# Performance work log

Measured on AMD Instinct MI355X. Metric: run time of the kernel, lower is better.

## Reference

```python
import jax, jax.numpy as jnp
import numpy as np

DIM = 1024
HEAD_DIM = 64
NUM_HEADS = DIM // HEAD_DIM
SCALE = HEAD_DIM ** -0.5
B, N, M = 2, 1024, 2048


def setup_inputs() -> dict:
    key = jax.random.key(0)
    ks = jax.random.split(key, 7)
    x = jax.random.normal(ks[0], (B, N, DIM), dtype=jnp.float32)
    context = jax.random.normal(ks[1], (B, M, DIM), dtype=jnp.float32)
    # query row has at least one valid key (avoids all -inf softmax rows).
    mask = jax.random.bernoulli(ks[2], 0.9, (B, N, M))
    mask = mask.at[:, :, 0].set(True)
    # Linear params (torch nn.Linear convention: y = x @ W.T + b)
    sq = (1.0 / DIM) ** 0.5
    Wq = jax.random.uniform(ks[3], (DIM, DIM), minval=-sq, maxval=sq, dtype=jnp.float32)
    Wkv = jax.random.uniform(ks[4], (2 * DIM, DIM), minval=-sq, maxval=sq, dtype=jnp.float32)
    b_kv = jax.random.uniform(ks[5], (2 * DIM,), minval=-sq, maxval=sq, dtype=jnp.float32)
    Wo = jax.random.uniform(ks[6], (DIM, DIM), minval=-sq, maxval=sq, dtype=jnp.float32)
    return {"x": x, "context": context, "mask": mask,
            "Wq": Wq, "Wkv": Wkv, "b_kv": b_kv, "Wo": Wo}


def reference(x, context, mask, Wq, Wkv, b_kv, Wo):
    b, n, c = x.shape
    m = context.shape[1]
    h, d = NUM_HEADS, HEAD_DIM
    # Q projection (no bias): [b, n, h, d] -> bhnd
    q = (x @ Wq.T).reshape(b, n, h, d).transpose(0, 2, 1, 3)
    # KV projection (with bias): [b, m, 2, h, d]
    kv = (context @ Wkv.T + b_kv).reshape(b, m, 2, h, d)
    k = kv[:, :, 0].transpose(0, 2, 1, 3)  # bhmd
    v = kv[:, :, 1].transpose(0, 2, 1, 3)  # bhmd
    # scores: bhnm, scale applied after matmul as in the original
    attn = jnp.einsum('bhnd,bhmd->bhnm', q, k) * SCALE
    attn = jnp.where(mask[:, None, :, :], attn, -jnp.inf)
    attn = jax.nn.softmax(attn, axis=-1)
    out = jnp.einsum('bhnm,bhmd->bhnd', attn, v)
    out = out.transpose(0, 2, 1, 3).reshape(b, n, h * d)
    return out @ Wo.T
```

## Files before the change

kernel.cpp:

```cpp
#include <hip/hip_runtime.h>


typedef __attribute__((ext_vector_type(8))) short short8;
typedef __attribute__((ext_vector_type(4))) short short4v;
typedef __attribute__((ext_vector_type(4))) float f32x4;
typedef __attribute__((ext_vector_type(4))) int int4v;

#define SCL2E 0.18033688011112042592f

__device__ __forceinline__ float bf2f(short s) {
  unsigned u = ((unsigned)(unsigned short)s) << 16;
  return __uint_as_float(u);
}
__device__ __forceinline__ short f2bf(float f) {
  unsigned u = __float_as_uint(f);
  u += 0x7fffu + ((u >> 16) & 1u);
  return (short)(u >> 16);
}
__device__ __forceinline__ int cvt_pk_bf16(float a, float b) {
  int r;
  asm("v_cvt_pk_bf16_f32 %0, %1, %2" : "=v"(r) : "v"(a), "v"(b));
  return r;
}
__device__ __forceinline__ void gld_lds16(const void* gp, void* lp) {
  __builtin_amdgcn_global_load_lds(
      (const __attribute__((address_space(1))) unsigned int*)gp,
      (__attribute__((address_space(3))) unsigned int*)lp, 16, 0, 0);
}
__device__ __forceinline__ void sbar() {
  __builtin_amdgcn_sched_barrier(0);
  __builtin_amdgcn_s_barrier();
  __builtin_amdgcn_sched_barrier(0);
}
#define WAITVM(N) asm volatile("s_waitcnt vmcnt(" #N ")" ::: "memory")

__device__ __forceinline__ void pipesync() {
  asm volatile("s_waitcnt vmcnt(0) lgkmcnt(0)" ::: "memory");
  __builtin_amdgcn_sched_barrier(0);
  __builtin_amdgcn_s_barrier();
  __builtin_amdgcn_sched_barrier(0);
}
__device__ __forceinline__ short4v cvt4(float4 v) {
  short4v o;
  o[0] = f2bf(v.x); o[1] = f2bf(v.y); o[2] = f2bf(v.z); o[3] = f2bf(v.w);
  return o;
}

__global__ __launch_bounds__(256) void prep(
    const unsigned char* __restrict__ mask, unsigned long long* __restrict__ pm,
    const float* __restrict__ Wq, const float* __restrict__ Wkv,
    const float* __restrict__ Wo, const float* __restrict__ x,
    const float* __restrict__ ctx, short* __restrict__ wqb,
    short* __restrict__ wkvb, short* __restrict__ wob,
    short* __restrict__ xb, short* __restrict__ ctxb) {
  const int row = blockIdx.x;
  const int wave = threadIdx.x >> 6, lane = threadIdx.x & 63;
  const unsigned char p8 = mask[lane * 4 + 1];
  const int p32 = ((const int*)mask)[lane * 2 + 1];
  const int shift =
      (__ballot(p8 != 0) != 0ull) ? 0 : ((__ballot(p32 != 0) != 0ull) ? 2 : 3);
  const size_t mbase = ((size_t)row * 2048) << shift;
#pragma unroll
  for (int j = 0; j < 8; j++) {
    const int c = wave * 512 + j * 64 + lane;
    const unsigned long long bits = __ballot(mask[mbase + ((size_t)c << shift)] != 0);
    if (lane == 0) pm[(size_t)row * 32 + wave * 8 + j] = bits;
  }
  const int gid = blockIdx.x * 256 + threadIdx.x;
  {
    const int T = gid * 4;
    const int j = T & 4, r15 = (T >> 3) & 15, q = (T >> 7) & 3;
    const int f = (T >> 9) & 7, kc = (T >> 12) & 31, rt = T >> 17;
    const int r = rt * 128 + f * 16 + r15, k = kc * 32 + q * 8 + j;
    *(short4v*)(xb + T) = cvt4(*(const float4*)(x + (((size_t)r) << 10) + k));
  }
#pragma unroll
  for (int it = 0; it < 2; it++) {
    const int T = (gid + it * 524288) * 4;
    const int j = T & 4, r15 = (T >> 3) & 15, q = (T >> 7) & 3;
    const int f = (T >> 9) & 7, kc = (T >> 12) & 31, rt = T >> 17;
    const int r = rt * 128 + f * 16 + r15, k = kc * 32 + q * 8 + j;
    *(short4v*)(ctxb + T) = cvt4(*(const float4*)(ctx + (((size_t)r) << 10) + k));
  }
  {
    const int T = gid * 4;
    const int j = T & 4, r15 = (T >> 3) & 15, q = (T >> 7) & 3;
    const int f = (T >> 9) & 7, kc = (T >> 12) & 31, rt = T >> 17;
    const int r = rt * 128 + f * 16 + r15, k = kc * 32 + q * 8 + j;
    *(short4v*)(wkvb + T) = cvt4(*(const float4*)(Wkv + (((size_t)r) << 10) + k));
  }
  if (gid < 262144) {
    const int T = gid * 4;
    {
      const int j = T & 4, r15 = (T >> 3) & 15, q = (T >> 7) & 3;
      const int f = (T >> 9) & 7, kc = (T >> 12) & 31, rt = T >> 17;
      const int r = rt * 128 + f * 16 + r15, k = kc * 32 + q * 8 + j;
      *(short4v*)(wqb + T) = cvt4(*(const float4*)(Wq + (((size_t)r) << 10) + k));
    }
    {
      const int j = T & 4, r15 = (T >> 3) & 15, q = (T >> 7) & 3;
      const int f = (T >> 9) & 3, kc = (T >> 11) & 31, rt = T >> 16;
      const int r = rt * 64 + f * 16 + r15, k = kc * 32 + q * 8 + j;
      *(short4v*)(wob + T) = cvt4(*(const float4*)(Wo + (((size_t)r) << 10) + k));
    }
  }
}

__global__ __launch_bounds__(256, 3)
void qkv_gemm(const short* __restrict__ xb, const short* __restrict__ ctxb,
              const short* __restrict__ wqb, const short* __restrict__ wkvb,
              const float* __restrict__ bias, short* __restrict__ qws,
              short* __restrict__ kws, short* __restrict__ vtws) {
  __shared__ __align__(16) short ldsA[3][4096];
  __shared__ __align__(16) short ldsB[3][4096];
  const int tid = threadIdx.x;
  const int wave = tid >> 6, lane = tid & 63;
  const int l15 = lane & 15, lg = lane >> 4;
  const int bx0 = blockIdx.x;
  const int bx = (bx0 & 7) * 80 + (bx0 >> 3);
  const bool isKV = bx < 512;
  const int rt = isKV ? (bx >> 4) : ((bx - 512) >> 3);
  const int ct = isKV ? (bx & 15) : ((bx - 512) & 7);
  const short* Amat = isKV ? ctxb : xb;
  const short* Bw = isKV ? wkvb : wqb;
  const int wr = wave >> 1, wc = wave & 1;

  f32x4 acc[4][4];
#pragma unroll
  for (int i = 0; i < 4; i++)
#pragma unroll
    for (int j = 0; j < 4; j++) acc[i][j] = (f32x4){0.f, 0.f, 0.f, 0.f};

  const short* ga0 = Amat + (size_t)rt * 131072 + wave * 512 + lane * 8;
  const short* ga1 = ga0 + 2048;
  const short* gb0 = Bw + (size_t)ct * 131072 + wave * 512 + lane * 8;
  const short* gb1 = gb0 + 2048;

  auto stage = [&](int kk, int buf) {
    const size_t koff = (size_t)kk * 4096;
    short* dA = &ldsA[buf][0];
    short* dB = &ldsB[buf][0];
    gld_lds16(ga0 + koff, dA + wave * 512);
    gld_lds16(ga1 + koff, dA + (wave + 4) * 512);
    gld_lds16(gb0 + koff, dB + wave * 512);
    gld_lds16(gb1 + koff, dB + (wave + 4) * 512);
  };
  auto compute = [&](int buf) {
    const short* sA = &ldsA[buf][0];
    const short* sB = &ldsB[buf][0];
    short8 af[4], bfr[4];
#pragma unroll
    for (int t = 0; t < 4; t++)
      af[t] = *(const short8*)&sA[((wr * 4 + t) * 64 + lane) * 8];
#pragma unroll
    for (int t = 0; t < 4; t++)
      bfr[t] = *(const short8*)&sB[((wc * 4 + t) * 64 + lane) * 8];
#pragma unroll
    for (int i = 0; i < 4; i++)
#pragma unroll
      for (int j = 0; j < 4; j++)
        acc[i][j] =
            __builtin_amdgcn_mfma_f32_16x16x32_bf16(af[i], bfr[j], acc[i][j], 0, 0, 0);
  };

  stage(0, 0);
  stage(1, 1);
  int cur = 0, nxt = 2;
  for (int i = 0; i < 30; ++i) {
    WAITVM(4);
    sbar();
    stage(i + 2, nxt);
    compute(cur);
    cur = (cur == 2) ? 0 : cur + 1;
    nxt = (nxt == 2) ? 0 : nxt + 1;
  }
  WAITVM(4);
  sbar();
  compute(cur);
  cur = (cur == 2) ? 0 : cur + 1;
  WAITVM(0);
  sbar();
  compute(cur);

#pragma unroll
  for (int i = 0; i < 4; i++)
#pragma unroll
    for (int j = 0; j < 4; j++)
#pragma unroll
      for (int r = 0; r < 4; r++) {
        const int gr = rt * 128 + wr * 64 + i * 16 + lg * 4 + r;
        const int gc = ct * 128 + wc * 64 + j * 16 + l15;
        float v = acc[i][j][r];
        if (isKV) {
          v += bias[gc];
          const int b = gr >> 11, m = gr & 2047;
          const int kv = gc >> 10, hh = (gc >> 6) & 15, d = gc & 63;
          if (kv == 0)
            kws[((((size_t)b * 16 + hh) * 2048 + m) << 6) + d] = f2bf(v);
          else {
            const int mp = (m & ~31) | (((m >> 2) & 3) << 3) |
                           (((m >> 4) & 1) << 2) | (m & 3);
            vtws[(((size_t)b * 16 + hh) * 64 + d) * 2048 + mp] = f2bf(v);
          }
        } else {
          const int b = gr >> 10, n = gr & 1023, hh = gc >> 6, d = gc & 63;
          qws[((((size_t)b * 16 + hh) * 1024 + n) << 6) + d] = f2bf(v * SCL2E);
        }
      }
}

__global__ __launch_bounds__(512, 4)
void attn_split(const short* __restrict__ Qg, const short* __restrict__ Kg,
                const short* __restrict__ Vtg,
                const unsigned int* __restrict__ pm,
                float* __restrict__ opart, float* __restrict__ lpart) {
  __shared__ __align__(16) short ldsK[2][8192];
  __shared__ __align__(16) short ldsV[2][8192];
  const int tid = threadIdx.x;
  const int w = tid >> 6, lane = tid & 63;
  const int l15 = lane & 15, lg = lane >> 4;
  const int bx = blockIdx.x;
  const int bhid = bx & 31, qt = (bx >> 5) & 7, half = bx >> 8;
  const int b = bhid >> 4, h = bhid & 15;
  const int n0 = qt * 128, m_base = half * 1024;
  const size_t bh = (size_t)b * 16 + h;
  const short* Qb = Qg + (bh * 1024 + n0) * 64;
  const short* Kb = Kg + (bh << 17);
  const short* Vb = Vtg + (bh << 17);
  const unsigned int* pmw =
      pm + ((size_t)(b * 1024 + n0 + w * 16 + l15) << 6) + (m_base >> 5);

  uint4 mku[8];
#pragma unroll
  for (int c = 0; c < 8; c++) mku[c] = *(const uint4*)(pmw + c * 4);

  auto stageKV = [&](int c, int buf) {
    const int m0 = m_base + c * 128;
    short* dK = &ldsK[buf][0];
    short* dV = &ldsV[buf][0];
#pragma unroll
    for (int ii = 0; ii < 2; ii++) {
      const int f = w * 2 + ii;
      const int t = f >> 1, ks = f & 1;
      gld_lds16(Kb + (size_t)(m0 + t * 16 + l15) * 64 + ks * 32 + lg * 8,
                dK + f * 512);
      const int vt = f >> 2, vk = f & 3;
      gld_lds16(Vb + (size_t)(vt * 16 + l15) * 2048 + (m0 + vk * 32 + lg * 8),
                dV + f * 512);
    }
  };

#pragma unroll
  for (int ii = 0; ii < 2; ii++)
    gld_lds16(Qb + (size_t)(w * 16 + l15) * 64 + ii * 32 + lg * 8,
              &ldsV[1][(w * 2 + ii) * 512]);
  stageKV(0, 0);
  pipesync();
  short8 qf[2];
#pragma unroll
  for (int ks = 0; ks < 2; ks++)
    qf[ks] = *(const short8*)&ldsV[1][((w * 2 + ks) * 64 + lane) * 8];
  asm volatile("s_waitcnt lgkmcnt(0)" ::: "memory");
  sbar();

  short8 onesf;
#pragma unroll
  for (int i = 0; i < 8; i++) onesf[i] = (short)0x3F80;

  f32x4 o[4], lacc;
#pragma unroll
  for (int ct = 0; ct < 4; ct++) o[ct] = (f32x4){0.f, 0.f, 0.f, 0.f};
  lacc = (f32x4){0.f, 0.f, 0.f, 0.f};
  const int sb = lg * 4;

  auto computeC = [&](uint4 mk, int buf) {
    const short* sK = &ldsK[buf][0];
    const short* sV = &ldsV[buf][0];
    int4v pw4[4];
#pragma unroll
    for (int h2 = 0; h2 < 2; h2++) {
      f32x4 s[4];
#pragma unroll
      for (int t2 = 0; t2 < 4; t2++) s[t2] = (f32x4){0.f, 0.f, 0.f, 0.f};
#pragma unroll
      for (int t2 = 0; t2 < 4; t2++) {
        const int t = h2 * 4 + t2;
#pragma unroll
        for (int ks = 0; ks < 2; ks++) {
          const short8 kf = *(const short8*)&sK[((t * 2 + ks) * 64 + lane) * 8];
          s[t2] = __builtin_amdgcn_mfma_f32_16x16x32_bf16(kf, qf[ks], s[t2], 0, 0, 0);
        }
      }
#pragma unroll
      for (int t2 = 0; t2 < 4; t2++) {
        const int t = h2 * 4 + t2;
        const unsigned int mw = ((t >> 1) == 0) ? mk.x
                              : ((t >> 1) == 1) ? mk.y
                              : ((t >> 1) == 2) ? mk.z : mk.w;
        float p[4];
#pragma unroll
        for (int r = 0; r < 4; r++) {
          const bool att = (mw >> (((t & 1) << 4) + sb + r)) & 1;
          p[r] = exp2f(att ? s[t2][r] : -1e30f);
        }
        pw4[t >> 1][(t & 1) * 2] = cvt_pk_bf16(p[0], p[1]);
        pw4[t >> 1][(t & 1) * 2 + 1] = cvt_pk_bf16(p[2], p[3]);
      }
    }
#pragma unroll
    for (int ks2 = 0; ks2 < 4; ks2++) {
      const short8 pf = __builtin_bit_cast(short8, pw4[ks2]);
#pragma unroll
      for (int ct = 0; ct < 4; ct++) {
        const short8 vf = *(const short8*)&sV[((ct * 4 + ks2) * 64 + lane) * 8];
        o[ct] = __builtin_amdgcn_mfma_f32_16x16x32_bf16(pf, vf, o[ct], 0, 0, 0);
      }
      lacc = __builtin_amdgcn_mfma_f32_16x16x32_bf16(pf, onesf, lacc, 0, 0, 0);
    }
  };

#pragma unroll
  for (int c = 0; c < 8; c++) {
    if (c + 1 < 8) {
      stageKV(c + 1, (c + 1) & 1);
      WAITVM(4);
    } else {
      WAITVM(0);
    }
    sbar();
    computeC(mku[c], c & 1);
    sbar();
  }

#pragma unroll
  for (int ct = 0; ct < 4; ct++)
#pragma unroll
    for (int r = 0; r < 4; r++) {
      const int n = n0 + w * 16 + lg * 4 + r;
      opart[((size_t)half << 21) + (((size_t)b * 1024 + n) << 10) + h * 64 +
            ct * 16 + l15] = o[ct][r];
    }
  if (l15 == 0) {
#pragma unroll
    for (int r = 0; r < 4; r++) {
      const int n = n0 + w * 16 + lg * 4 + r;
      lpart[((size_t)half << 15) + bh * 1024 + n] = lacc[r];
    }
  }
}

__global__ __launch_bounds__(256) void combine(
    const float* __restrict__ opart, const float* __restrict__ lpart,
    short* __restrict__ aoT) {
  const int gid = blockIdx.x * 256 + threadIdx.x;
  const int T = gid * 4;
  const int j = T & 4, r15 = (T >> 3) & 15, q = (T >> 7) & 3;
  const int f = (T >> 9) & 3, kc = (T >> 11) & 31, rt = T >> 16;
  const int row = rt * 64 + f * 16 + r15;
  const int col = kc * 32 + q * 8 + j;
  const int b = row >> 10, n = row & 1023, h = col >> 6;
  const size_t src = (((size_t)row) << 10) + col;
  const float4 o1 = *(const float4*)(opart + src);
  const float4 o2 = *(const float4*)(opart + (1u << 21) + src);
  const float l1 = lpart[(size_t)(b * 16 + h) * 1024 + n];
  const float l2 = lpart[(1u << 15) + (size_t)(b * 16 + h) * 1024 + n];
  const float inv = 1.f / fmaxf(l1 + l2, 1e-30f);
  short4v o;
  o[0] = f2bf((o1.x + o2.x) * inv); o[1] = f2bf((o1.y + o2.y) * inv);
  o[2] = f2bf((o1.z + o2.z) * inv); o[3] = f2bf((o1.w + o2.w) * inv);
  *(short4v*)(aoT + T) = o;
}

__global__ __launch_bounds__(256, 3)
void o_gemm(const short* __restrict__ aoT, const short* __restrict__ wobT,
            float* __restrict__ Of) {
  __shared__ __align__(16) short ldsA[3][4096];
  __shared__ __align__(16) short ldsB[3][4096];
  const int tid = threadIdx.x;
  const int w = tid >> 6, lane = tid & 63;
  const int l15 = lane & 15, lg = lane >> 4;
  const int bx0 = blockIdx.x;
  const int bx = (bx0 & 7) * 64 + (bx0 >> 3);
  const int rt = bx >> 4, ct = bx & 15;

  f32x4 acc[4];
#pragma unroll
  for (int j = 0; j < 4; j++) acc[j] = (f32x4){0.f, 0.f, 0.f, 0.f};

  const short* ga = aoT + (size_t)rt * 65536 + w * 512 + lane * 8;
  const short* gb = wobT + (size_t)ct * 65536 + w * 512 + lane * 8;

  auto stage = [&](int t, int buf) {
    const size_t koff = (size_t)t * 4096;
    gld_lds16(ga + koff, &ldsA[buf][0] + w * 512);
    gld_lds16(ga + koff + 2048, &ldsA[buf][0] + 2048 + w * 512);
    gld_lds16(gb + koff, &ldsB[buf][0] + w * 512);
    gld_lds16(gb + koff + 2048, &ldsB[buf][0] + 2048 + w * 512);
  };
  auto compute = [&](int buf) {
    const short* sA = &ldsA[buf][0];
    const short* sB = &ldsB[buf][0];
    const short8 af0 = *(const short8*)&sA[(w * 64 + lane) * 8];
    const short8 af1 = *(const short8*)&sA[2048 + (w * 64 + lane) * 8];
#pragma unroll
    for (int j = 0; j < 4; j++) {
      const short8 bf0 = *(const short8*)&sB[(j * 64 + lane) * 8];
      const short8 bf1 = *(const short8*)&sB[2048 + (j * 64 + lane) * 8];
      acc[j] = __builtin_amdgcn_mfma_f32_16x16x32_bf16(af0, bf0, acc[j], 0, 0, 0);
      acc[j] = __builtin_amdgcn_mfma_f32_16x16x32_bf16(af1, bf1, acc[j], 0, 0, 0);
    }
  };

  stage(0, 0);
  stage(1, 1);
#pragma unroll
  for (int i = 0; i < 14; ++i) {
    WAITVM(4);
    sbar();
    stage(i + 2, (i + 2) % 3);
    compute(i % 3);
  }
  WAITVM(4);
  sbar();
  compute(14 % 3);
  WAITVM(0);
  sbar();
  compute(15 % 3);

#pragma unroll
  for (int j = 0; j < 4; j++)
#pragma unroll
    for (int r = 0; r < 4; r++) {
      const int gr = rt * 64 + w * 16 + lg * 4 + r;
      const int gc = ct * 64 + j * 16 + l15;
      Of[(size_t)gr * 1024 + gc] = acc[j][r];
    }
}

extern "C" void kernel_launch(void* const* d_in, const int* in_sizes, int n_in,
                              void* d_out, int out_size, void* d_ws, size_t ws_size,
                              hipStream_t stream) {
  const float* x   = (const float*)d_in[0];
  const float* ctx = (const float*)d_in[1];
  const unsigned char* mask = (const unsigned char*)d_in[2];
  const float* Wq  = (const float*)d_in[3];
  const float* Wkv = (const float*)d_in[4];
  const float* bkv = (const float*)d_in[5];
  const float* Wo  = (const float*)d_in[6];
  float* out = (float*)d_out;

  char* wsb = (char*)d_ws;
  short* qws  = (short*)(wsb);
  short* kws  = (short*)(wsb + (4u << 20));
  short* vtws = (short*)(wsb + (12u << 20));
  short* wqb  = (short*)(wsb + (20u << 20));
  short* wkvb = (short*)(wsb + (22u << 20));
  short* wob  = (short*)(wsb + (26u << 20));
  unsigned long long* pmws = (unsigned long long*)(wsb + (28u << 20));
  float* opart = (float*)(wsb + (29u << 20));
  float* lpart = (float*)(wsb + (45u << 20));
  short* xb   = (short*)(wsb + (29u << 20));
  short* ctxb = (short*)(wsb + (33u << 20));
  short* ao = (short*)(wsb + (20u << 20));

  prep<<<2048, 256, 0, stream>>>(mask, pmws, Wq, Wkv, Wo, x, ctx,
                                 wqb, wkvb, wob, xb, ctxb);
  qkv_gemm<<<640, 256, 0, stream>>>(xb, ctxb, wqb, wkvb, bkv, qws, kws, vtws);
  attn_split<<<512, 512, 0, stream>>>(qws, kws, vtws, (const unsigned int*)pmws,
                                      opart, lpart);
  combine<<<2048, 256, 0, stream>>>(opart, lpart, ao);
  o_gemm<<<512, 256, 0, stream>>>(ao, wob, out);
}
```

Baseline: 205.4 us.

## Triple-buffer 64-key KV chunks with one barrier per step and MFMA priority

Halves the KV chunk size to 64 keys and replaces the double buffer with a three-deep LDS ring. Loads are issued two chunks ahead right after a single barrier, so the trailing barrier per iteration is gone. Wraps the MFMA sections in s_setprio to favour matrix issue across waves. The ring also shrinks LDS use, which may allow more occupancy, at the cost of more loop iterations, more barriers in total and smaller per-chunk work.

```diff
diff --git a/kernel.cpp b/kernel.cpp
--- a/kernel.cpp
+++ b/kernel.cpp
@@ -5,6 +5,7 @@
 typedef __attribute__((ext_vector_type(4))) short short4v;
 typedef __attribute__((ext_vector_type(4))) float f32x4;
 typedef __attribute__((ext_vector_type(4))) int int4v;
+typedef __attribute__((ext_vector_type(2))) int int2v;
 
 #define SCL2E 0.18033688011112042592f
 
@@ -214,8 +215,8 @@
                 const short* __restrict__ Vtg,
                 const unsigned int* __restrict__ pm,
                 float* __restrict__ opart, float* __restrict__ lpart) {
-  __shared__ __align__(16) short ldsK[2][8192];
-  __shared__ __align__(16) short ldsV[2][8192];
+  __shared__ __align__(16) short ldsK[3][4096];
+  __shared__ __align__(16) short ldsV[3][4096];
   const int tid = threadIdx.x;
   const int w = tid >> 6, lane = tid & 63;
   const int l15 = lane & 15, lg = lane >> 4;
@@ -232,36 +233,37 @@
 
   uint4 mku[8];
 #pragma unroll
-  for (int c = 0; c < 8; c++) mku[c] = *(const uint4*)(pmw + c * 4);
+  for (int i = 0; i < 8; i++) mku[i] = *(const uint4*)(pmw + i * 4);
 
   auto stageKV = [&](int c, int buf) {
-    const int m0 = m_base + c * 128;
-    short* dK = &ldsK[buf][0];
-    short* dV = &ldsV[buf][0];
-#pragma unroll
-    for (int ii = 0; ii < 2; ii++) {
-      const int f = w * 2 + ii;
-      const int t = f >> 1, ks = f & 1;
-      gld_lds16(Kb + (size_t)(m0 + t * 16 + l15) * 64 + ks * 32 + lg * 8,
-                dK + f * 512);
-      const int vt = f >> 2, vk = f & 3;
-      gld_lds16(Vb + (size_t)(vt * 16 + l15) * 2048 + (m0 + vk * 32 + lg * 8),
-                dV + f * 512);
-    }
-  };
-
-#pragma unroll
-  for (int ii = 0; ii < 2; ii++)
-    gld_lds16(Qb + (size_t)(w * 16 + l15) * 64 + ii * 32 + lg * 8,
-              &ldsV[1][(w * 2 + ii) * 512]);
+    const int m0 = m_base + c * 64;
+    const int t = w >> 1, ks = w & 1;
+    gld_lds16(Kb + (size_t)(m0 + t * 16 + l15) * 64 + ks * 32 + lg * 8,
+              &ldsK[buf][w * 512]);
+    const int vt = w >> 1, vk = w & 1;
+    gld_lds16(Vb + (size_t)(vt * 16 + l15) * 2048 + (m0 + vk * 32 + lg * 8),
+              &ldsV[buf][w * 512]);
+  };
+
+#pragma unroll
+  for (int ii = 0; ii < 2; ii++) {
+    const int f = w * 2 + ii;
+    const int t = f >> 1, ks = f & 1;
+    short* dst = (f < 8) ? &ldsK[1][f * 512] : &ldsK[2][(f - 8) * 512];
+    gld_lds16(Qb + (size_t)(t * 16 + l15) * 64 + ks * 32 + lg * 8, dst);
+  }
   stageKV(0, 0);
   pipesync();
   short8 qf[2];
 #pragma unroll
-  for (int ks = 0; ks < 2; ks++)
-    qf[ks] = *(const short8*)&ldsV[1][((w * 2 + ks) * 64 + lane) * 8];
+  for (int ks = 0; ks < 2; ks++) {
+    const int f = w * 2 + ks;
+    const short* src = (f < 8) ? &ldsK[1][f * 512] : &ldsK[2][(f - 8) * 512];
+    qf[ks] = *(const short8*)&src[lane * 8];
+  }
   asm volatile("s_waitcnt lgkmcnt(0)" ::: "memory");
   sbar();
+  stageKV(1, 1);
 
   short8 onesf;
 #pragma unroll
@@ -273,63 +275,107 @@
   lacc = (f32x4){0.f, 0.f, 0.f, 0.f};
   const int sb = lg * 4;
 
-  auto computeC = [&](uint4 mk, int buf) {
+  auto computeC = [&](unsigned int mw0, unsigned int mw1, int buf) {
     const short* sK = &ldsK[buf][0];
     const short* sV = &ldsV[buf][0];
-    int4v pw4[4];
-#pragma unroll
-    for (int h2 = 0; h2 < 2; h2++) {
-      f32x4 s[4];
-#pragma unroll
-      for (int t2 = 0; t2 < 4; t2++) s[t2] = (f32x4){0.f, 0.f, 0.f, 0.f};
-#pragma unroll
-      for (int t2 = 0; t2 < 4; t2++) {
-        const int t = h2 * 4 + t2;
-#pragma unroll
-        for (int ks = 0; ks < 2; ks++) {
-          const short8 kf = *(const short8*)&sK[((t * 2 + ks) * 64 + lane) * 8];
-          s[t2] = __builtin_amdgcn_mfma_f32_16x16x32_bf16(kf, qf[ks], s[t2], 0, 0, 0);
-        }
-      }
-#pragma unroll
-      for (int t2 = 0; t2 < 4; t2++) {
-        const int t = h2 * 4 + t2;
-        const unsigned int mw = ((t >> 1) == 0) ? mk.x
-                              : ((t >> 1) == 1) ? mk.y
-                              : ((t >> 1) == 2) ? mk.z : mk.w;
-        float p[4];
-#pragma unroll
-        for (int r = 0; r < 4; r++) {
-          const bool att = (mw >> (((t & 1) << 4) + sb + r)) & 1;
-          p[r] = exp2f(att ? s[t2][r] : -1e30f);
-        }
-        pw4[t >> 1][(t & 1) * 2] = cvt_pk_bf16(p[0], p[1]);
-        pw4[t >> 1][(t & 1) * 2 + 1] = cvt_pk_bf16(p[2], p[3]);
-      }
-    }
-#pragma unroll
-    for (int ks2 = 0; ks2 < 4; ks2++) {
+    f32x4 s[4];
+#pragma unroll
+    for (int t = 0; t < 4; t++) s[t] = (f32x4){0.f, 0.f, 0.f, 0.f};
+    __builtin_amdgcn_s_setprio(1);
+#pragma unroll
+    for (int t = 0; t < 4; t++)
+#pragma unroll
+      for (int ks = 0; ks < 2; ks++) {
+        const short8 kf = *(const short8*)&sK[((t * 2 + ks) * 64 + lane) * 8];
+        s[t] = __builtin_amdgcn_mfma_f32_16x16x32_bf16(kf, qf[ks], s[t], 0, 0, 0);
+      }
+    __builtin_amdgcn_s_setprio(0);
+    int2v pw[2];
+#pragma unroll
+    for (int t = 0; t < 4; t++) {
+      const unsigned int mw = (t >> 1) ? mw1 : mw0;
+      float p[4];
+#pragma unroll
+      for (int r = 0; r < 4; r++) {
+        const bool att = (mw >> (((t & 1) << 4) + sb + r)) & 1;
+        p[r] = exp2f(att ? s[t][r] : -1e30f);
+      }
+      pw[t >> 1][(t & 1) * 2] = cvt_pk_bf16(p[0], p[1]);
+      pw[t >> 1][(t & 1) * 2 + 1] = cvt_pk_bf16(p[2], p[3]);
+    }
+    __builtin_amdgcn_s_setprio(1);
+#pragma unroll
+    for (int ks2 = 0; ks2 < 2; ks2++) {
+      int4v pwf;
+      pwf[0] = pw[ks2][0]; pwf[1] = pw[ks2][1];
+      pwf[2] = pw[ks2][2]; pwf[3] = pw[ks2][3];
+      const short8 pf = __builtin_bit_cast(short8, pwf);
+#pragma unroll
+      for (int ct = 0; ct < 4; ct++) {
+        const short8 vf = *(const short8*)&sV[((ct * 2 + ks2) * 64 + lane) * 8];
+        o[ct] = __builtin_amdgcn_mfma_f32_16x16x32_bf16(pf, vf, o[ct], 0, 0, 0);
+      }
+      lacc = __builtin_amdgcn_mfma_f32_16x16x32_bf16(pf, onesf, lacc, 0, 0, 0);
+    }
+    __builtin_amdgcn_s_setprio(0);
+  };
+  (void)computeC;
+
+  auto computeC4 = [&](unsigned int mw0, unsigned int mw1, int buf) {
+    const short* sK = &ldsK[buf][0];
+    const short* sV = &ldsV[buf][0];
+    f32x4 s[4];
+#pragma unroll
+    for (int t = 0; t < 4; t++) s[t] = (f32x4){0.f, 0.f, 0.f, 0.f};
+    __builtin_amdgcn_s_setprio(1);
+#pragma unroll
+    for (int t = 0; t < 4; t++)
+#pragma unroll
+      for (int ks = 0; ks < 2; ks++) {
+        const short8 kf = *(const short8*)&sK[((t * 2 + ks) * 64 + lane) * 8];
+        s[t] = __builtin_amdgcn_mfma_f32_16x16x32_bf16(kf, qf[ks], s[t], 0, 0, 0);
+      }
+    __builtin_amdgcn_s_setprio(0);
+    int4v pw4[2];
+#pragma unroll
+    for (int t = 0; t < 4; t++) {
+      const unsigned int mw = (t >> 1) ? mw1 : mw0;
+      float p[4];
+#pragma unroll
+      for (int r = 0; r < 4; r++) {
+        const bool att = (mw >> (((t & 1) << 4) + sb + r)) & 1;
+        p[r] = exp2f(att ? s[t][r] : -1e30f);
+      }
+      pw4[t >> 1][(t & 1) * 2] = cvt_pk_bf16(p[0], p[1]);
+      pw4[t >> 1][(t & 1) * 2 + 1] = cvt_pk_bf16(p[2], p[3]);
+    }
+    __builtin_amdgcn_s_setprio(1);
+#pragma unroll
+    for (int ks2 = 0; ks2 < 2; ks2++) {
       const short8 pf = __builtin_bit_cast(short8, pw4[ks2]);
 #pragma unroll
       for (int ct = 0; ct < 4; ct++) {
-        const short8 vf = *(const short8*)&sV[((ct * 4 + ks2) * 64 + lane) * 8];
+        const short8 vf = *(const short8*)&sV[((ct * 2 + ks2) * 64 + lane) * 8];
         o[ct] = __builtin_amdgcn_mfma_f32_16x16x32_bf16(pf, vf, o[ct], 0, 0, 0);
       }
       lacc = __builtin_amdgcn_mfma_f32_16x16x32_bf16(pf, onesf, lacc, 0, 0, 0);
     }
-  };
-
-#pragma unroll
-  for (int c = 0; c < 8; c++) {
-    if (c + 1 < 8) {
-      stageKV(c + 1, (c + 1) & 1);
-      WAITVM(4);
+    __builtin_amdgcn_s_setprio(0);
+  };
+
+#pragma unroll
+  for (int c = 0; c < 16; c++) {
+    if (c < 15) {
+      WAITVM(2);
     } else {
       WAITVM(0);
     }
     sbar();
-    computeC(mku[c], c & 1);
-    sbar();
+    if (c + 2 < 16) stageKV(c + 2, (c + 2) % 3);
+    const uint4 mk = mku[c >> 1];
+    const unsigned int mw0 = (c & 1) ? mk.z : mk.x;
+    const unsigned int mw1 = (c & 1) ? mk.w : mk.y;
+    computeC4(mw0, mw1, c % 3);
   }
 
 #pragma unroll
```

Measured after the change: 209.0 us. Within noise of the previous version (+1.8%).

## Fuse split-KV combine into attention kernel via intra-block LDS reduction

Applied to the files above, without the earlier changes.

The attention kernel now assigns both key halves of a 64-query tile to two wave groups inside one block, each streaming 64-key chunks. The partial outputs and row sums are then reduced through LDS and written directly in the o_gemm tiled bf16 layout. This removes the separate combine kernel and its fp32 partial-output round trip through global memory. In exchange each block covers fewer queries per K/V chunk, so K/V loads are amortised over fewer rows and the loop runs more iterations with more barriers.

```diff
diff --git a/kernel.cpp b/kernel.cpp
--- a/kernel.cpp
+++ b/kernel.cpp
@@ -8,10 +8,6 @@
 
 #define SCL2E 0.18033688011112042592f
 
-__device__ __forceinline__ float bf2f(short s) {
-  unsigned u = ((unsigned)(unsigned short)s) << 16;
-  return __uint_as_float(u);
-}
 __device__ __forceinline__ short f2bf(float f) {
   unsigned u = __float_as_uint(f);
   u += 0x7fffu + ((u >> 16) & 1u);
@@ -44,6 +40,10 @@
   short4v o;
   o[0] = f2bf(v.x); o[1] = f2bf(v.y); o[2] = f2bf(v.z); o[3] = f2bf(v.w);
   return o;
+}
+__device__ __forceinline__ size_t off64(int row, int k) {
+  return ((size_t)(((row >> 6) * 32 + (k >> 5)) * 4 + ((row >> 4) & 3)) << 9) +
+         (((((k >> 3) & 3) * 16 + (row & 15)) << 3) + (k & 7));
 }
 
 __global__ __launch_bounds__(256) void prep(
@@ -210,56 +210,56 @@
 }
 
 __global__ __launch_bounds__(512, 4)
-void attn_split(const short* __restrict__ Qg, const short* __restrict__ Kg,
+void attn_fused(const short* __restrict__ Qg, const short* __restrict__ Kg,
                 const short* __restrict__ Vtg,
                 const unsigned int* __restrict__ pm,
-                float* __restrict__ opart, float* __restrict__ lpart) {
+                short* __restrict__ aoT) {
   __shared__ __align__(16) short ldsK[2][8192];
   __shared__ __align__(16) short ldsV[2][8192];
   const int tid = threadIdx.x;
   const int w = tid >> 6, lane = tid & 63;
   const int l15 = lane & 15, lg = lane >> 4;
+  const int g = w >> 2, ww = w & 3;
   const int bx = blockIdx.x;
-  const int bhid = bx & 31, qt = (bx >> 5) & 7, half = bx >> 8;
+  const int bhid = bx & 31, qt = bx >> 5;
   const int b = bhid >> 4, h = bhid & 15;
-  const int n0 = qt * 128, m_base = half * 1024;
+  const int n0 = qt * 64, m_base = g * 1024;
   const size_t bh = (size_t)b * 16 + h;
   const short* Qb = Qg + (bh * 1024 + n0) * 64;
   const short* Kb = Kg + (bh << 17);
   const short* Vb = Vtg + (bh << 17);
   const unsigned int* pmw =
-      pm + ((size_t)(b * 1024 + n0 + w * 16 + l15) << 6) + (m_base >> 5);
+      pm + ((size_t)(b * 1024 + n0 + ww * 16 + l15) << 6) + (m_base >> 5);
 
   uint4 mku[8];
 #pragma unroll
-  for (int c = 0; c < 8; c++) mku[c] = *(const uint4*)(pmw + c * 4);
+  for (int i = 0; i < 8; i++) mku[i] = *(const uint4*)(pmw + i * 4);
 
   auto stageKV = [&](int c, int buf) {
-    const int m0 = m_base + c * 128;
-    short* dK = &ldsK[buf][0];
-    short* dV = &ldsV[buf][0];
+    const int m0 = m_base + c * 64;
+    short* dK = &ldsK[buf][g * 4096];
+    short* dV = &ldsV[buf][g * 4096];
 #pragma unroll
     for (int ii = 0; ii < 2; ii++) {
-      const int f = w * 2 + ii;
-      const int t = f >> 1, ks = f & 1;
-      gld_lds16(Kb + (size_t)(m0 + t * 16 + l15) * 64 + ks * 32 + lg * 8,
-                dK + f * 512);
-      const int vt = f >> 2, vk = f & 3;
-      gld_lds16(Vb + (size_t)(vt * 16 + l15) * 2048 + (m0 + vk * 32 + lg * 8),
-                dV + f * 512);
-    }
-  };
-
-#pragma unroll
-  for (int ii = 0; ii < 2; ii++)
-    gld_lds16(Qb + (size_t)(w * 16 + l15) * 64 + ii * 32 + lg * 8,
-              &ldsV[1][(w * 2 + ii) * 512]);
+      gld_lds16(Kb + (size_t)(m0 + ww * 16 + l15) * 64 + ii * 32 + lg * 8,
+                dK + (ww * 2 + ii) * 512);
+      gld_lds16(Vb + (size_t)(ww * 16 + l15) * 2048 + (m0 + ii * 32 + lg * 8),
+                dV + (ww * 2 + ii) * 512);
+    }
+  };
+
+  if (g == 0) {
+#pragma unroll
+    for (int ii = 0; ii < 2; ii++)
+      gld_lds16(Qb + (size_t)(ww * 16 + l15) * 64 + ii * 32 + lg * 8,
+                &ldsV[1][(ww * 2 + ii) * 512]);
+  }
   stageKV(0, 0);
   pipesync();
   short8 qf[2];
 #pragma unroll
   for (int ks = 0; ks < 2; ks++)
-    qf[ks] = *(const short8*)&ldsV[1][((w * 2 + ks) * 64 + lane) * 8];
+    qf[ks] = *(const short8*)&ldsV[1][((ww * 2 + ks) * 64 + lane) * 8];
   asm volatile("s_waitcnt lgkmcnt(0)" ::: "memory");
   sbar();
 
@@ -273,46 +273,38 @@
   lacc = (f32x4){0.f, 0.f, 0.f, 0.f};
   const int sb = lg * 4;
 
-  auto computeC = [&](uint4 mk, int buf) {
-    const short* sK = &ldsK[buf][0];
-    const short* sV = &ldsV[buf][0];
-    int4v pw4[4];
-#pragma unroll
-    for (int h2 = 0; h2 < 2; h2++) {
-      f32x4 s[4];
-#pragma unroll
-      for (int t2 = 0; t2 < 4; t2++) s[t2] = (f32x4){0.f, 0.f, 0.f, 0.f};
-#pragma unroll
-      for (int t2 = 0; t2 < 4; t2++) {
-        const int t = h2 * 4 + t2;
-#pragma unroll
-        for (int ks = 0; ks < 2; ks++) {
-          const short8 kf = *(const short8*)&sK[((t * 2 + ks) * 64 + lane) * 8];
-          s[t2] = __builtin_amdgcn_mfma_f32_16x16x32_bf16(kf, qf[ks], s[t2], 0, 0, 0);
-        }
+  auto computeC4 = [&](unsigned int mw0, unsigned int mw1, int buf) {
+    const short* sK = &ldsK[buf][g * 4096];
+    const short* sV = &ldsV[buf][g * 4096];
+    f32x4 s[4];
+#pragma unroll
+    for (int t = 0; t < 4; t++) s[t] = (f32x4){0.f, 0.f, 0.f, 0.f};
+#pragma unroll
+    for (int t = 0; t < 4; t++)
+#pragma unroll
+      for (int ks = 0; ks < 2; ks++) {
+        const short8 kf = *(const short8*)&sK[((t * 2 + ks) * 64 + lane) * 8];
+        s[t] = __builtin_amdgcn_mfma_f32_16x16x32_bf16(kf, qf[ks], s[t], 0, 0, 0);
       }
-#pragma unroll
-      for (int t2 = 0; t2 < 4; t2++) {
-        const int t = h2 * 4 + t2;
-        const unsigned int mw = ((t >> 1) == 0) ? mk.x
-                              : ((t >> 1) == 1) ? mk.y
-                              : ((t >> 1) == 2) ? mk.z : mk.w;
-        float p[4];
-#pragma unroll
-        for (int r = 0; r < 4; r++) {
-          const bool att = (mw >> (((t & 1) << 4) + sb + r)) & 1;
-          p[r] = exp2f(att ? s[t2][r] : -1e30f);
-        }
-        pw4[t >> 1][(t & 1) * 2] = cvt_pk_bf16(p[0], p[1]);
-        pw4[t >> 1][(t & 1) * 2 + 1] = cvt_pk_bf16(p[2], p[3]);
+    int4v pw4[2];
+#pragma unroll
+    for (int t = 0; t < 4; t++) {
+      const unsigned int mw = (t >> 1) ? mw1 : mw0;
+      float p[4];
+#pragma unroll
+      for (int r = 0; r < 4; r++) {
+        const bool att = (mw >> (((t & 1) << 4) + sb + r)) & 1;
+        p[r] = exp2f(att ? s[t][r] : -1e30f);
       }
-    }
-#pragma unroll
-    for (int ks2 = 0; ks2 < 4; ks2++) {
+      pw4[t >> 1][(t & 1) * 2] = cvt_pk_bf16(p[0], p[1]);
+      pw4[t >> 1][(t & 1) * 2 + 1] = cvt_pk_bf16(p[2], p[3]);
+    }
+#pragma unroll
+    for (int ks2 = 0; ks2 < 2; ks2++) {
       const short8 pf = __builtin_bit_cast(short8, pw4[ks2]);
 #pragma unroll
       for (int ct = 0; ct < 4; ct++) {
-        const short8 vf = *(const short8*)&sV[((ct * 4 + ks2) * 64 + lane) * 8];
+        const short8 vf = *(const short8*)&sV[((ct * 2 + ks2) * 64 + lane) * 8];
         o[ct] = __builtin_amdgcn_mfma_f32_16x16x32_bf16(pf, vf, o[ct], 0, 0, 0);
       }
       lacc = __builtin_amdgcn_mfma_f32_16x16x32_bf16(pf, onesf, lacc, 0, 0, 0);
@@ -320,55 +312,52 @@
   };
 
 #pragma unroll
-  for (int c = 0; c < 8; c++) {
-    if (c + 1 < 8) {
+  for (int c = 0; c < 16; c++) {
+    if (c + 1 < 16) {
       stageKV(c + 1, (c + 1) & 1);
       WAITVM(4);
     } else {
       WAITVM(0);
     }
     sbar();
-    computeC(mku[c], c & 1);
+    const uint4 mk = mku[c >> 1];
+    const unsigned int mw0 = (c & 1) ? mk.z : mk.x;
+    const unsigned int mw1 = (c & 1) ? mk.w : mk.y;
+    computeC4(mw0, mw1, c & 1);
     sbar();
   }
 
-#pragma unroll
-  for (int ct = 0; ct < 4; ct++)
+  float* fO = (float*)&ldsK[0][0];
+  float* fL = (float*)&ldsV[0][0];
+  if (g == 1) {
+#pragma unroll
+    for (int ct = 0; ct < 4; ct++)
+#pragma unroll
+      for (int r = 0; r < 4; r++)
+        fO[(ww * 64 + lane) * 16 + ct * 4 + r] = o[ct][r];
+#pragma unroll
+    for (int r = 0; r < 4; r++) fL[(ww * 64 + lane) * 4 + r] = lacc[r];
+  }
+  asm volatile("s_waitcnt lgkmcnt(0)" ::: "memory");
+  sbar();
+  if (g == 0) {
+    float inv[4];
 #pragma unroll
     for (int r = 0; r < 4; r++) {
-      const int n = n0 + w * 16 + lg * 4 + r;
-      opart[((size_t)half << 21) + (((size_t)b * 1024 + n) << 10) + h * 64 +
-            ct * 16 + l15] = o[ct][r];
-    }
-  if (l15 == 0) {
-#pragma unroll
-    for (int r = 0; r < 4; r++) {
-      const int n = n0 + w * 16 + lg * 4 + r;
-      lpart[((size_t)half << 15) + bh * 1024 + n] = lacc[r];
-    }
-  }
-}
-
-__global__ __launch_bounds__(256) void combine(
-    const float* __restrict__ opart, const float* __restrict__ lpart,
-    short* __restrict__ aoT) {
-  const int gid = blockIdx.x * 256 + threadIdx.x;
-  const int T = gid * 4;
-  const int j = T & 4, r15 = (T >> 3) & 15, q = (T >> 7) & 3;
-  const int f = (T >> 9) & 3, kc = (T >> 11) & 31, rt = T >> 16;
-  const int row = rt * 64 + f * 16 + r15;
-  const int col = kc * 32 + q * 8 + j;
-  const int b = row >> 10, n = row & 1023, h = col >> 6;
-  const size_t src = (((size_t)row) << 10) + col;
-  const float4 o1 = *(const float4*)(opart + src);
-  const float4 o2 = *(const float4*)(opart + (1u << 21) + src);
-  const float l1 = lpart[(size_t)(b * 16 + h) * 1024 + n];
-  const float l2 = lpart[(1u << 15) + (size_t)(b * 16 + h) * 1024 + n];
-  const float inv = 1.f / fmaxf(l1 + l2, 1e-30f);
-  short4v o;
-  o[0] = f2bf((o1.x + o2.x) * inv); o[1] = f2bf((o1.y + o2.y) * inv);
-  o[2] = f2bf((o1.z + o2.z) * inv); o[3] = f2bf((o1.w + o2.w) * inv);
-  *(short4v*)(aoT + T) = o;
+      const float lt = lacc[r] + fL[(ww * 64 + lane) * 4 + r];
+      inv[r] = 1.f / fmaxf(lt, 1e-30f);
+    }
+#pragma unroll
+    for (int ct = 0; ct < 4; ct++)
+#pragma unroll
+      for (int r = 0; r < 4; r++) {
+        const float v =
+            (o[ct][r] + fO[(ww * 64 + lane) * 16 + ct * 4 + r]) * inv[r];
+        const int row = b * 1024 + n0 + ww * 16 + lg * 4 + r;
+        const int col = h * 64 + ct * 16 + l15;
+        aoT[off64(row, col)] = f2bf(v);
+      }
+  }
 }
 
 __global__ __launch_bounds__(256, 3)
@@ -457,17 +446,14 @@
   short* wkvb = (short*)(wsb + (22u << 20));
   short* wob  = (short*)(wsb + (26u << 20));
   unsigned long long* pmws = (unsigned long long*)(wsb + (28u << 20));
-  float* opart = (float*)(wsb + (29u << 20));
-  float* lpart = (float*)(wsb + (45u << 20));
   short* xb   = (short*)(wsb + (29u << 20));
   short* ctxb = (short*)(wsb + (33u << 20));
-  short* ao = (short*)(wsb + (20u << 20));
+  short* ao = (short*)(wsb + (41u << 20));
 
   prep<<<2048, 256, 0, stream>>>(mask, pmws, Wq, Wkv, Wo, x, ctx,
                                  wqb, wkvb, wob, xb, ctxb);
   qkv_gemm<<<640, 256, 0, stream>>>(xb, ctxb, wqb, wkvb, bkv, qws, kws, vtws);
-  attn_split<<<512, 512, 0, stream>>>(qws, kws, vtws, (const unsigned int*)pmws,
-                                      opart, lpart);
-  combine<<<2048, 256, 0, stream>>>(opart, lpart, ao);
+  attn_fused<<<512, 512, 0, stream>>>(qws, kws, vtws,
+                                      (const unsigned int*)pmws, ao);
   o_gemm<<<512, 256, 0, stream>>>(ao, wob, out);
 }
```

After: 208.4 us. About the same (+1.5%).

## Stage bf16 conversion through LDS for coalesced tiled writes; raise MFMA priority

Applied to the files above, without the earlier changes.

The prep kernel used to convert fp32 inputs and weights to bf16 with per-thread scattered gathers into the MFMA-tiled layout. It now assigns each block a 64x128 tile, does coalesced float4 reads, converts into padded LDS, and writes contiguous 16-byte chunks in the tiled layout. This is meant to cut uncoalesced global reads, at the cost of an LDS round trip and a barrier. Separately, s_setprio brackets the MFMA sections of the attention inner loop so waves issuing matrix ops get scheduling priority over waves doing exp and mask work.

```diff
diff --git a/kernel.cpp b/kernel.cpp
--- a/kernel.cpp
+++ b/kernel.cpp
@@ -8,10 +8,6 @@
 
 #define SCL2E 0.18033688011112042592f
 
-__device__ __forceinline__ float bf2f(short s) {
-  unsigned u = ((unsigned)(unsigned short)s) << 16;
-  return __uint_as_float(u);
-}
 __device__ __forceinline__ short f2bf(float f) {
   unsigned u = __float_as_uint(f);
   u += 0x7fffu + ((u >> 16) & 1u);
@@ -44,6 +40,10 @@
   short4v o;
   o[0] = f2bf(v.x); o[1] = f2bf(v.y); o[2] = f2bf(v.z); o[3] = f2bf(v.w);
   return o;
+}
+__device__ __forceinline__ size_t off64(int row, int k) {
+  return ((size_t)(((row >> 6) * 32 + (k >> 5)) * 4 + ((row >> 4) & 3)) << 9) +
+         (((((k >> 3) & 3) * 16 + (row & 15)) << 3) + (k & 7));
 }
 
 __global__ __launch_bounds__(256) void prep(
@@ -53,6 +53,7 @@
     const float* __restrict__ ctx, short* __restrict__ wqb,
     short* __restrict__ wkvb, short* __restrict__ wob,
     short* __restrict__ xb, short* __restrict__ ctxb) {
+  __shared__ __align__(16) short lds[64][136];
   const int row = blockIdx.x;
   const int wave = threadIdx.x >> 6, lane = threadIdx.x & 63;
   const unsigned char p8 = mask[lane * 4 + 1];
@@ -66,43 +67,44 @@
     const unsigned long long bits = __ballot(mask[mbase + ((size_t)c << shift)] != 0);
     if (lane == 0) pm[(size_t)row * 32 + wave * 8 + j] = bits;
   }
-  const int gid = blockIdx.x * 256 + threadIdx.x;
-  {
-    const int T = gid * 4;
-    const int j = T & 4, r15 = (T >> 3) & 15, q = (T >> 7) & 3;
-    const int f = (T >> 9) & 7, kc = (T >> 12) & 31, rt = T >> 17;
-    const int r = rt * 128 + f * 16 + r15, k = kc * 32 + q * 8 + j;
-    *(short4v*)(xb + T) = cvt4(*(const float4*)(x + (((size_t)r) << 10) + k));
-  }
-#pragma unroll
-  for (int it = 0; it < 2; it++) {
-    const int T = (gid + it * 524288) * 4;
-    const int j = T & 4, r15 = (T >> 3) & 15, q = (T >> 7) & 3;
-    const int f = (T >> 9) & 7, kc = (T >> 12) & 31, rt = T >> 17;
-    const int r = rt * 128 + f * 16 + r15, k = kc * 32 + q * 8 + j;
-    *(short4v*)(ctxb + T) = cvt4(*(const float4*)(ctx + (((size_t)r) << 10) + k));
-  }
-  {
-    const int T = gid * 4;
-    const int j = T & 4, r15 = (T >> 3) & 15, q = (T >> 7) & 3;
-    const int f = (T >> 9) & 7, kc = (T >> 12) & 31, rt = T >> 17;
-    const int r = rt * 128 + f * 16 + r15, k = kc * 32 + q * 8 + j;
-    *(short4v*)(wkvb + T) = cvt4(*(const float4*)(Wkv + (((size_t)r) << 10) + k));
-  }
-  if (gid < 262144) {
-    const int T = gid * 4;
-    {
-      const int j = T & 4, r15 = (T >> 3) & 15, q = (T >> 7) & 3;
-      const int f = (T >> 9) & 7, kc = (T >> 12) & 31, rt = T >> 17;
-      const int r = rt * 128 + f * 16 + r15, k = kc * 32 + q * 8 + j;
-      *(short4v*)(wqb + T) = cvt4(*(const float4*)(Wq + (((size_t)r) << 10) + k));
-    }
-    {
-      const int j = T & 4, r15 = (T >> 3) & 15, q = (T >> 7) & 3;
-      const int f = (T >> 9) & 3, kc = (T >> 11) & 31, rt = T >> 16;
-      const int r = rt * 64 + f * 16 + r15, k = kc * 32 + q * 8 + j;
-      *(short4v*)(wob + T) = cvt4(*(const float4*)(Wo + (((size_t)r) << 10) + k));
-    }
+
+  const int bid = blockIdx.x;
+  if (bid >= 1280) return;
+  const float* src;
+  short* dst;
+  int cb;
+  bool t64 = false;
+  if (bid < 256) {
+    src = x; dst = xb; cb = bid;
+  } else if (bid < 768) {
+    src = ctx; dst = ctxb; cb = bid - 256;
+  } else if (bid < 1024) {
+    src = Wkv; dst = wkvb; cb = bid - 768;
+  } else if (bid < 1152) {
+    src = Wq; dst = wqb; cb = bid - 1024;
+  } else {
+    src = Wo; dst = wob; cb = bid - 1152; t64 = true;
+  }
+  const int R0 = (cb >> 3) * 64, C0 = (cb & 7) * 128;
+  const int t = threadIdx.x;
+#pragma unroll
+  for (int p = 0; p < 8; p++) {
+    const int r = R0 + p * 8 + (t >> 5), c = C0 + (t & 31) * 4;
+    const float4 v = *(const float4*)(src + (size_t)r * 1024 + c);
+    *(short4v*)&lds[p * 8 + (t >> 5)][(t & 31) * 4] = cvt4(v);
+  }
+  __syncthreads();
+  const int rt = t64 ? (R0 >> 6) : (R0 >> 7);
+  const int f0 = t64 ? 0 : ((R0 >> 6) & 1) * 4;
+  const int fl = t >> 6, q = (t >> 4) & 3, r15 = t & 15;
+  const int lrow = fl * 16 + r15;
+#pragma unroll
+  for (int kc_l = 0; kc_l < 4; kc_l++) {
+    const int kc = (C0 >> 5) + kc_l;
+    const size_t base = t64 ? ((size_t)((rt * 32 + kc) * 4)) * 512
+                            : ((size_t)((rt * 32 + kc) * 8 + f0)) * 512;
+    const short8 vv = *(const short8*)&lds[lrow][kc_l * 32 + q * 8];
+    *(short8*)(dst + base + t * 8) = vv;
   }
 }
 
@@ -282,6 +284,7 @@
       f32x4 s[4];
 #pragma unroll
       for (int t2 = 0; t2 < 4; t2++) s[t2] = (f32x4){0.f, 0.f, 0.f, 0.f};
+      __builtin_amdgcn_s_setprio(1);
 #pragma unroll
       for (int t2 = 0; t2 < 4; t2++) {
         const int t = h2 * 4 + t2;
@@ -291,6 +294,7 @@
           s[t2] = __builtin_amdgcn_mfma_f32_16x16x32_bf16(kf, qf[ks], s[t2], 0, 0, 0);
         }
       }
+      __builtin_amdgcn_s_setprio(0);
 #pragma unroll
       for (int t2 = 0; t2 < 4; t2++) {
         const int t = h2 * 4 + t2;
@@ -307,6 +311,7 @@
         pw4[t >> 1][(t & 1) * 2 + 1] = cvt_pk_bf16(p[2], p[3]);
       }
     }
+    __builtin_amdgcn_s_setprio(1);
 #pragma unroll
     for (int ks2 = 0; ks2 < 4; ks2++) {
       const short8 pf = __builtin_bit_cast(short8, pw4[ks2]);
@@ -317,6 +322,7 @@
       }
       lacc = __builtin_amdgcn_mfma_f32_16x16x32_bf16(pf, onesf, lacc, 0, 0, 0);
     }
+    __builtin_amdgcn_s_setprio(0);
   };
 
 #pragma unroll
```

Result: no change. 202.4 us (median of 2 runs) (-1.4%).
